# Kernel tuning notes

Measured on AMD Instinct MI355X. Metric: run time of the kernel, lower is better.

## Reference

```python
import jax, jax.numpy as jnp
import numpy as np

B, N, NF, DEG = 128, 1024, 64, 16
NH = 128          # top-level n_hidden
H = NH // 2       # per-branch hidden (64)
NNODES = B * N
NEDGES = NNODES * DEG
ANG = 2


def _lin(key, fi, fo):
    k1, k2 = jax.random.split(key)
    s = 1.0 / np.sqrt(fi)
    return (jax.random.uniform(k1, (fi, fo), minval=-s, maxval=s, dtype=jnp.float32),
            jax.random.uniform(k2, (fo,), minval=-s, maxval=s, dtype=jnp.float32))

_PARAM_DEFS = [("W_pre1_a", "b_pre1_a", NF, H), ("W_pre2_a", "b_pre2_a", H, H), ("W_gcn_a", "b_gcn_a", H, H),
               ("W_pre1_b", "b_pre1_b", NF, H), ("W_pre2_b", "b_pre2_b", H, H), ("W_gcn_b", "b_gcn_b", H, H),
               ("W_lin1", "b_lin1", 2 * NH + 1, NH), ("W_lin2", "b_lin2", NH, NH // 2),
               ("W_lin3", "b_lin3", NH // 2, 1), ("W_cb", "b_cb", NH // 2, 1),
               ("W_om", "b_om", NH // 2, ANG), ("W_th", "b_th", NH // 2, ANG), ("W_ph", "b_ph", NH // 2, ANG)]


def setup_inputs() -> dict:
    key = jax.random.key(0)
    ks = jax.random.split(key, 24)

    def edges(k):
        # block-structured edges: each graph g owns nodes [g*N, (g+1)*N)
        e = jax.random.randint(k, (2, NEDGES), 0, N, dtype=jnp.int32)
        off = (jnp.arange(NEDGES, dtype=jnp.int32) // (N * DEG)) * N
        return e + off[None, :]

    batch = jnp.arange(NNODES, dtype=jnp.int32) // N
    inp = {
        "x_a": jax.random.normal(ks[0], (NNODES, NF), dtype=jnp.float32),
        "edge_index_a": edges(ks[1]),
        "edge_attr_a": jax.random.uniform(ks[2], (NEDGES,), dtype=jnp.float32),
        "x_a_batch": batch,
        "x_b": jax.random.normal(ks[3], (NNODES, NF), dtype=jnp.float32),
        "edge_index_b": edges(ks[4]),
        "edge_attr_b": jax.random.uniform(ks[5], (NEDGES,), dtype=jnp.float32),
        "x_b_batch": batch,
        "linker_size": jax.random.uniform(ks[6], (B, 1), dtype=jnp.float32),
    }
    for i, (wn, bn, fi, fo) in enumerate(_PARAM_DEFS):
        w, b = _lin(ks[7 + i], fi, fo)
        inp[wn] = w
        inp[bn] = b
    return inp


def _gcn(x, W, b, src, dst, ew, n):
    # GCNConv with edge weights and self loops (fill_value=1):
    #   out = D^{-1/2} (A + I) D^{-1/2} (x W) + b
    h = x @ W
    deg = jax.ops.segment_sum(ew, dst, num_segments=n) + 1.0
    dinv = jax.lax.rsqrt(deg)
    norm = dinv[src] * ew * dinv[dst]                        # [E]
    out = jax.ops.segment_sum(h[src] * norm[:, None], dst, num_segments=n)
    out = out + h * (dinv * dinv)[:, None]                   # self-loop contribution
    return out + b


def _branch(x, ei, ea, bat, Wp1, bp1, Wp2, bp2, Wg, bg):
    x = jax.nn.relu(x @ Wp1 + bp1)
    x = jax.nn.relu(x @ Wp2 + bp2)
    x = jax.nn.relu(_gcn(x, Wg, bg, ei[0], ei[1], ea, x.shape[0]))
    s = jax.ops.segment_sum(x, bat, num_segments=B)          # gsp: global sum pool
    cnt = jax.ops.segment_sum(jnp.ones((x.shape[0], 1), x.dtype), bat, num_segments=B)
    return jnp.concatenate([s, s / cnt], axis=1)             # [B, 2H] = [gsp || gap(mean)]


def reference(x_a, edge_index_a, edge_attr_a, x_a_batch,
              x_b, edge_index_b, edge_attr_b, x_b_batch, linker_size,
              W_pre1_a, b_pre1_a, W_pre2_a, b_pre2_a, W_gcn_a, b_gcn_a,
              W_pre1_b, b_pre1_b, W_pre2_b, b_pre2_b, W_gcn_b, b_gcn_b,
              W_lin1, b_lin1, W_lin2, b_lin2, W_lin3, b_lin3,
              W_cb, b_cb, W_om, b_om, W_th, b_th, W_ph, b_ph):
    xa = _branch(x_a, edge_index_a, edge_attr_a, x_a_batch,
                 W_pre1_a, b_pre1_a, W_pre2_a, b_pre2_a, W_gcn_a, b_gcn_a)
    xb = _branch(x_b, edge_index_b, edge_attr_b, x_b_batch,
                 W_pre1_b, b_pre1_b, W_pre2_b, b_pre2_b, W_gcn_b, b_gcn_b)
    x = jnp.concatenate([xa, xb, linker_size], axis=1)       # [B, 2*NH+1]
    x = jax.nn.relu(x @ W_lin1 + b_lin1)                     # dropout p=0.0 -> identity
    x = jax.nn.relu(x @ W_lin2 + b_lin2)
    ca = x @ W_lin3 + b_lin3                                 # loss_type='bce' -> no sigmoid
    cb = x @ W_cb + b_cb
    om = x @ W_om + b_om
    th = x @ W_th + b_th
    ph = x @ W_ph + b_ph
    return (ca, cb, om, th, ph)
```

## Files before the change

kernel.cpp:

```cpp
#include <hip/hip_runtime.h>
#include <hip/hip_bf16.h>

#define NNODES 131072
#define NEDGES 2097152
#define NB     128
#define NPG    1024
#define EPG    16384

#define OFF_DEG      0
#define OFF_POOLED   (OFF_DEG + 2*NNODES)
#define OFF_WT       (OFF_POOLED + 2*NB*64)
#define OFF_H        (OFF_WT + 6*4096)
#define OFF_CNT      (OFF_H + (size_t)2*NNODES*64)
#define OFF_ROWSTART (OFF_CNT + 2*NNODES)
#define OFF_CURSOR   (OFF_ROWSTART + 2*NNODES)
#define OFF_CSR      (OFF_CURSOR + 2*NNODES)
#define WS_NEEDED    ((OFF_CSR + (size_t)4*NEDGES) * 4)

#define CSRB_LDS 145408

typedef __attribute__((ext_vector_type(8))) short bfrag;
typedef __attribute__((ext_vector_type(4))) float f32x4;

__device__ __forceinline__ unsigned short f2bf(float v) {
    unsigned int u = __float_as_uint(v);
    unsigned int r = (u + 0x7fffu + ((u >> 16) & 1u)) >> 16;
    return (unsigned short)r;
}
__device__ __forceinline__ float bf2f(unsigned short s) {
    return __uint_as_float(((unsigned int)s) << 16);
}
__device__ __forceinline__ float2 ntload2(const float2* p) {
    unsigned long long u = __builtin_nontemporal_load(
        reinterpret_cast<const unsigned long long*>(p));
    float2 r;
    r.x = __uint_as_float((unsigned int)(u & 0xffffffffu));
    r.y = __uint_as_float((unsigned int)(u >> 32));
    return r;
}

__global__ void wprep(const float* __restrict__ w0, const float* __restrict__ w1,
                      const float* __restrict__ w2, const float* __restrict__ w3,
                      const float* __restrict__ w4, const float* __restrict__ w5,
                      unsigned short* __restrict__ wf) {
    int m = blockIdx.x;
    const float* w = (m == 0) ? w0 : (m == 1) ? w1 : (m == 2) ? w2
                   : (m == 3) ? w3 : (m == 4) ? w4 : w5;
    for (int idx = threadIdx.x; idx < 4096; idx += blockDim.x) {
        int ft   = idx >> 10;
        int kt   = (idx >> 9) & 1;
        int lane = (idx >> 3) & 63;
        int i    = idx & 7;
        int f = ft * 16 + (lane & 15);
        int k = kt * 32 + ((lane >> 4) << 3) + i;
        float v = w[k * 64 + f];
        unsigned short hi = f2bf(v);
        unsigned short lo = f2bf(v - bf2f(hi));
        wf[m * 8192 + idx]        = hi;
        wf[m * 8192 + 4096 + idx] = lo;
    }
}

__global__ __launch_bounds__(512) void csr_build2(
    const int* __restrict__ eia, const float* __restrict__ eaa,
    const int* __restrict__ eib, const float* __restrict__ eab,
    float* __restrict__ deg, int* __restrict__ rowstart,
    int* __restrict__ cnt, float2* __restrict__ csr) {
    extern __shared__ char smem[];
    float2* scsr = (float2*)smem;
    float*  sdeg = (float*)(smem + 131072);
    int*    scnt = (int*)(smem + 135168);
    int*    scur = (int*)(smem + 139264);
    int*    sm   = (int*)(smem + 143360);
    const int g  = blockIdx.x;
    const int br = blockIdx.y;
    const int* ei   = br ? eib : eia;
    const float* ea = br ? eab : eaa;
    const int t     = threadIdx.x;
    const int ebase = g * EPG;
    const int nbase = g * NPG;

    for (int i = t; i < NPG; i += 512) { sdeg[i] = 0.f; scnt[i] = 0; }
    __syncthreads();

#pragma unroll 4
    for (int it = 0; it < EPG / 512; ++it) {
        int e = ebase + it * 512 + t;
        int d = ei[NEDGES + e] - nbase;
        float w = ea[e];
        atomicAdd(&scnt[d], 1);
        atomicAdd(&sdeg[d], w);
    }
    __syncthreads();

    for (int i = t; i < NPG; i += 512) {
        float dv = sdeg[i];
        deg[br * NNODES + nbase + i] = dv;
        sdeg[i] = rsqrtf(dv + 1.f);
    }

    int c0 = scnt[t * 2 + 0], c1 = scnt[t * 2 + 1];
    int T = c0 + c1;
    sm[t] = T;
    __syncthreads();
    for (int off = 1; off < 512; off <<= 1) {
        int v = (t >= off) ? sm[t - off] : 0;
        __syncthreads();
        sm[t] += v;
        __syncthreads();
    }
    int excl = sm[t] - T;
    int r0 = excl, r1 = excl + c0;
    int nout = br * NNODES + nbase + t * 2;
    rowstart[nout + 0] = ebase + r0;
    rowstart[nout + 1] = ebase + r1;
    cnt[nout + 0] = c0; cnt[nout + 1] = c1;
    scur[t * 2 + 0] = r0; scur[t * 2 + 1] = r1;
    __syncthreads();

#pragma unroll 4
    for (int it = 0; it < EPG / 512; ++it) {
        int e = ebase + it * 512 + t;
        int srcg = ei[e];
        int s = srcg - nbase;
        int d = ei[NEDGES + e] - nbase;
        float w = ea[e];
        int pos = atomicAdd(&scur[d], 1);
        float2 pr;
        pr.x = __int_as_float(srcg);
        pr.y = sdeg[s] * w * sdeg[d];
        scsr[pos] = pr;
    }
    __syncthreads();

    float4* dst4 = (float4*)(csr + (size_t)br * NEDGES + ebase);
    const float4* src4 = (const float4*)scsr;
    for (int i = t; i < 8192; i += 512) dst4[i] = src4[i];
}

__global__ __launch_bounds__(256) void csr_build(
    const int* __restrict__ eia, const float* __restrict__ eaa,
    const int* __restrict__ eib, const float* __restrict__ eab,
    float* __restrict__ deg, int* __restrict__ rowstart,
    int* __restrict__ cnt, float2* __restrict__ csr) {
    __shared__ float sdeg[NPG];
    __shared__ int   scnt[NPG];
    __shared__ int   scur[NPG];
    __shared__ int   sm[256];
    const int g  = blockIdx.x;
    const int br = blockIdx.y;
    const int* ei   = br ? eib : eia;
    const float* ea = br ? eab : eaa;
    const int t     = threadIdx.x;
    const int ebase = g * EPG;
    const int nbase = g * NPG;

    for (int i = t; i < NPG; i += 256) { sdeg[i] = 0.f; scnt[i] = 0; }
    __syncthreads();
#pragma unroll 4
    for (int it = 0; it < EPG / 256; ++it) {
        int e = ebase + it * 256 + t;
        int d = ei[NEDGES + e] - nbase;
        float w = ea[e];
        atomicAdd(&scnt[d], 1);
        atomicAdd(&sdeg[d], w);
    }
    __syncthreads();
    for (int i = t; i < NPG; i += 256) {
        float dv = sdeg[i];
        deg[br * NNODES + nbase + i] = dv;
        sdeg[i] = rsqrtf(dv + 1.f);
    }
    int c0 = scnt[t * 4 + 0], c1 = scnt[t * 4 + 1], c2 = scnt[t * 4 + 2], c3 = scnt[t * 4 + 3];
    int T = c0 + c1 + c2 + c3;
    sm[t] = T;
    __syncthreads();
    for (int off = 1; off < 256; off <<= 1) {
        int v = (t >= off) ? sm[t - off] : 0;
        __syncthreads();
        sm[t] += v;
        __syncthreads();
    }
    int excl = sm[t] - T;
    int base = ebase + excl;
    int r0 = base, r1 = base + c0, r2 = r1 + c1, r3 = r2 + c2;
    int nout = br * NNODES + nbase + t * 4;
    rowstart[nout + 0] = r0; rowstart[nout + 1] = r1;
    rowstart[nout + 2] = r2; rowstart[nout + 3] = r3;
    cnt[nout + 0] = c0; cnt[nout + 1] = c1; cnt[nout + 2] = c2; cnt[nout + 3] = c3;
    scur[t * 4 + 0] = r0; scur[t * 4 + 1] = r1;
    scur[t * 4 + 2] = r2; scur[t * 4 + 3] = r3;
    __syncthreads();
    float2* cso = csr + (size_t)br * NEDGES;
#pragma unroll 4
    for (int it = 0; it < EPG / 256; ++it) {
        int e = ebase + it * 256 + t;
        int srcg = ei[e];
        int s = srcg - nbase;
        int d = ei[NEDGES + e] - nbase;
        float w = ea[e];
        int pos = atomicAdd(&scur[d], 1);
        float2 pr;
        pr.x = __int_as_float(srcg);
        pr.y = sdeg[s] * w * sdeg[d];
        cso[pos] = pr;
    }
}

__global__ __launch_bounds__(256) void node_mlp_mfma(
    const float* __restrict__ xa, const float* __restrict__ xb,
    const unsigned short* __restrict__ wf,
    const float* __restrict__ b1a, const float* __restrict__ b2a,
    const float* __restrict__ b1b, const float* __restrict__ b2b,
    unsigned short* __restrict__ hout) {
    __shared__ float lds[4 * 16 * 65];
    const int br = blockIdx.y;
    const float* x = br ? xb : xa;
    const unsigned short* wfb = wf + br * 3 * 8192;
    const float* b1 = br ? b1b : b1a;
    const float* b2 = br ? b2b : b2a;
    const int wave = threadIdx.x >> 6;
    const int lane = threadIdx.x & 63;
    const int row  = lane & 15;
    const int kg   = lane >> 4;
    const int n0   = blockIdx.x * 64 + wave * 16;
    float* wlds = &lds[wave * 16 * 65];

    bfrag ahi[2], alo[2];
#pragma unroll
    for (int kt = 0; kt < 2; ++kt) {
        const float4* p = reinterpret_cast<const float4*>(
            x + (size_t)(n0 + row) * 64 + kt * 32 + kg * 8);
        float4 v0 = p[0], v1 = p[1];
        float vv[8] = {v0.x, v0.y, v0.z, v0.w, v1.x, v1.y, v1.z, v1.w};
        bfrag h, l;
#pragma unroll
        for (int i = 0; i < 8; ++i) {
            unsigned short hb = f2bf(vv[i]);
            unsigned short lb = f2bf(vv[i] - bf2f(hb));
            h[i] = (short)hb;
            l[i] = (short)lb;
        }
        ahi[kt] = h; alo[kt] = l;
    }

#pragma unroll
    for (int layer = 0; layer < 3; ++layer) {
        const unsigned short* wl = wfb + layer * 8192;
        bfrag bhi[4][2], blo[4][2];
#pragma unroll
        for (int ft = 0; ft < 4; ++ft)
#pragma unroll
            for (int kt = 0; kt < 2; ++kt) {
                bhi[ft][kt] = *reinterpret_cast<const bfrag*>(wl + ft * 1024 + kt * 512 + lane * 8);
                blo[ft][kt] = *reinterpret_cast<const bfrag*>(wl + 4096 + ft * 1024 + kt * 512 + lane * 8);
            }
        f32x4 acc[4];
#pragma unroll
        for (int ft = 0; ft < 4; ++ft) {
            float bv = (layer == 0) ? b1[ft * 16 + row]
                     : (layer == 1) ? b2[ft * 16 + row] : 0.f;
            acc[ft] = (f32x4){bv, bv, bv, bv};
        }
#pragma unroll
        for (int ft = 0; ft < 4; ++ft)
#pragma unroll
            for (int kt = 0; kt < 2; ++kt) {
                acc[ft] = __builtin_amdgcn_mfma_f32_16x16x32_bf16(ahi[kt], bhi[ft][kt], acc[ft], 0, 0, 0);
                acc[ft] = __builtin_amdgcn_mfma_f32_16x16x32_bf16(alo[kt], bhi[ft][kt], acc[ft], 0, 0, 0);
                acc[ft] = __builtin_amdgcn_mfma_f32_16x16x32_bf16(ahi[kt], blo[ft][kt], acc[ft], 0, 0, 0);
            }

        if (layer < 2) {
#pragma unroll
            for (int ft = 0; ft < 4; ++ft)
#pragma unroll
                for (int r = 0; r < 4; ++r)
                    wlds[(kg * 4 + r) * 65 + ft * 16 + row] = fmaxf(acc[ft][r], 0.f);
            __syncthreads();
#pragma unroll
            for (int kt = 0; kt < 2; ++kt) {
                const float* rp = &wlds[row * 65 + kt * 32 + kg * 8];
                bfrag h, l;
#pragma unroll
                for (int i = 0; i < 8; ++i) {
                    float v = rp[i];
                    unsigned short hb = f2bf(v);
                    unsigned short lb = f2bf(v - bf2f(hb));
                    h[i] = (short)hb;
                    l[i] = (short)lb;
                }
                ahi[kt] = h; alo[kt] = l;
            }
            __syncthreads();
        } else {
            unsigned short* hp = hout + (size_t)br * NNODES * 64 + (size_t)n0 * 64;
#pragma unroll
            for (int ft = 0; ft < 4; ++ft)
#pragma unroll
                for (int r = 0; r < 4; ++r)
                    hp[(kg * 4 + r) * 64 + ft * 16 + row] = f2bf(acc[ft][r]);
        }
    }
}

__global__ __launch_bounds__(256) void gcn_gather_pool(
    const int* __restrict__ rowstart, const int* __restrict__ cnt,
    const float2* __restrict__ csr, const float* __restrict__ deg,
    const unsigned short* __restrict__ h,
    const float* __restrict__ bga, const float* __restrict__ bgb,
    float* __restrict__ pooled) {
    __shared__ float red[256];
    const int bid  = blockIdx.x;
    const int xcd  = bid & 7;
    const int sub  = bid >> 3;
    const int gb   = xcd * 32 + (sub >> 4);
    const int blk  = sub & 15;
    const int br   = gb >> 7;
    const int g    = gb & 127;
    const int wave = threadIdx.x >> 6;
    const int lane = threadIdx.x & 63;
    const int n0   = g * NPG + blk * 64 + wave * 16;

    const int*    rs = rowstart + br * NNODES;
    const int*    ct = cnt + br * NNODES;
    const float2* cs = csr + (size_t)br * NEDGES;
    const float*  dg = deg + br * NNODES;
    const unsigned short* hh = h + (size_t)br * NNODES * 64;
    const float bias = (br ? bgb : bga)[lane];

    float psum = 0.f;
    for (int j = 0; j < 16; ++j) {
        int n = n0 + j;
        int r = __builtin_amdgcn_readfirstlane(rs[n]);
        int c = __builtin_amdgcn_readfirstlane(ct[n]);
        float s0 = 0.f, s1 = 0.f, s2 = 0.f, s3 = 0.f;
        float s4 = 0.f, s5 = 0.f, s6 = 0.f, s7 = 0.f;
        int i = 0;
        for (; i + 8 <= c; i += 8) {
            float2 p0 = ntload2(cs + r + i + 0);
            float2 p1 = ntload2(cs + r + i + 1);
            float2 p2 = ntload2(cs + r + i + 2);
            float2 p3 = ntload2(cs + r + i + 3);
            float2 p4 = ntload2(cs + r + i + 4);
            float2 p5 = ntload2(cs + r + i + 5);
            float2 p6 = ntload2(cs + r + i + 6);
            float2 p7 = ntload2(cs + r + i + 7);
            s0 = fmaf(p0.y, bf2f(hh[(size_t)__float_as_int(p0.x) * 64 + lane]), s0);
            s1 = fmaf(p1.y, bf2f(hh[(size_t)__float_as_int(p1.x) * 64 + lane]), s1);
            s2 = fmaf(p2.y, bf2f(hh[(size_t)__float_as_int(p2.x) * 64 + lane]), s2);
            s3 = fmaf(p3.y, bf2f(hh[(size_t)__float_as_int(p3.x) * 64 + lane]), s3);
            s4 = fmaf(p4.y, bf2f(hh[(size_t)__float_as_int(p4.x) * 64 + lane]), s4);
            s5 = fmaf(p5.y, bf2f(hh[(size_t)__float_as_int(p5.x) * 64 + lane]), s5);
            s6 = fmaf(p6.y, bf2f(hh[(size_t)__float_as_int(p6.x) * 64 + lane]), s6);
            s7 = fmaf(p7.y, bf2f(hh[(size_t)__float_as_int(p7.x) * 64 + lane]), s7);
        }
        for (; i + 4 <= c; i += 4) {
            float2 p0 = ntload2(cs + r + i + 0);
            float2 p1 = ntload2(cs + r + i + 1);
            float2 p2 = ntload2(cs + r + i + 2);
            float2 p3 = ntload2(cs + r + i + 3);
            s0 = fmaf(p0.y, bf2f(hh[(size_t)__float_as_int(p0.x) * 64 + lane]), s0);
            s1 = fmaf(p1.y, bf2f(hh[(size_t)__float_as_int(p1.x) * 64 + lane]), s1);
            s2 = fmaf(p2.y, bf2f(hh[(size_t)__float_as_int(p2.x) * 64 + lane]), s2);
            s3 = fmaf(p3.y, bf2f(hh[(size_t)__float_as_int(p3.x) * 64 + lane]), s3);
        }
        for (; i < c; ++i) {
            float2 p = ntload2(cs + r + i);
            s0 = fmaf(p.y, bf2f(hh[(size_t)__float_as_int(p.x) * 64 + lane]), s0);
        }
        float d = dg[n] + 1.f;
        float v = ((s0 + s1) + (s2 + s3)) + ((s4 + s5) + (s6 + s7))
                + bf2f(hh[(size_t)n * 64 + lane]) * (1.f / d) + bias;
        psum += fmaxf(v, 0.f);
    }
    red[threadIdx.x] = psum;
    __syncthreads();
    if (wave == 0) {
        float s = red[lane] + red[64 + lane] + red[128 + lane] + red[192 + lane];
        unsafeAtomicAdd(&pooled[br * (NB * 64) + g * 64 + lane], s);
    }
}

__global__ __launch_bounds__(128) void final_mlp(
    const float* __restrict__ pooled, const float* __restrict__ linker,
    const float* __restrict__ W1, const float* __restrict__ b1,
    const float* __restrict__ W2, const float* __restrict__ b2,
    const float* __restrict__ W3, const float* __restrict__ b3,
    const float* __restrict__ Wcb, const float* __restrict__ bcb,
    const float* __restrict__ Wom, const float* __restrict__ bom,
    const float* __restrict__ Wth, const float* __restrict__ bth,
    const float* __restrict__ Wph, const float* __restrict__ bph,
    float* __restrict__ out) {
    __shared__ float inv[260];
    __shared__ float x1[128];
    __shared__ float x2[64];
    const int g = blockIdx.x;
    const int t = threadIdx.x;
    if (t < 64) {
        float pa = pooled[g * 64 + t];
        float pb = pooled[NB * 64 + g * 64 + t];
        inv[t]       = pa;
        inv[64 + t]  = pa * (1.f / 1024.f);
        inv[128 + t] = pb;
        inv[192 + t] = pb * (1.f / 1024.f);
    }
    if (t == 0) inv[256] = linker[g];
    __syncthreads();

    {
        float a = b1[t];
        for (int i = 0; i < 257; ++i) a = fmaf(inv[i], W1[i * 128 + t], a);
        x1[t] = fmaxf(a, 0.f);
    }
    __syncthreads();
    if (t < 64) {
        float a = b2[t];
        for (int i = 0; i < 128; ++i) a = fmaf(x1[i], W2[i * 64 + t], a);
        x2[t] = fmaxf(a, 0.f);
    }
    __syncthreads();
    if (t < 8) {
        if (t == 0) {
            float a = b3[0];
            for (int i = 0; i < 64; ++i) a = fmaf(x2[i], W3[i], a);
            out[g] = a;
        } else if (t == 1) {
            float a = bcb[0];
            for (int i = 0; i < 64; ++i) a = fmaf(x2[i], Wcb[i], a);
            out[128 + g] = a;
        } else if (t < 4) {
            int j = t - 2; float a = bom[j];
            for (int i = 0; i < 64; ++i) a = fmaf(x2[i], Wom[i * 2 + j], a);
            out[256 + g * 2 + j] = a;
        } else if (t < 6) {
            int j = t - 4; float a = bth[j];
            for (int i = 0; i < 64; ++i) a = fmaf(x2[i], Wth[i * 2 + j], a);
            out[512 + g * 2 + j] = a;
        } else {
            int j = t - 6; float a = bph[j];
            for (int i = 0; i < 64; ++i) a = fmaf(x2[i], Wph[i * 2 + j], a);
            out[768 + g * 2 + j] = a;
        }
    }
}

extern "C" void kernel_launch(void* const* d_in, const int* in_sizes, int n_in,
                              void* d_out, int out_size, void* d_ws, size_t ws_size,
                              hipStream_t stream) {
    const float* x_a  = (const float*)d_in[0];
    const int*   ei_a = (const int*)d_in[1];
    const float* ea_a = (const float*)d_in[2];
    const float* x_b  = (const float*)d_in[4];
    const int*   ei_b = (const int*)d_in[5];
    const float* ea_b = (const float*)d_in[6];
    const float* linker = (const float*)d_in[8];
    const float* W_pre1_a = (const float*)d_in[9];
    const float* b_pre1_a = (const float*)d_in[10];
    const float* W_pre2_a = (const float*)d_in[11];
    const float* b_pre2_a = (const float*)d_in[12];
    const float* W_gcn_a  = (const float*)d_in[13];
    const float* b_gcn_a  = (const float*)d_in[14];
    const float* W_pre1_b = (const float*)d_in[15];
    const float* b_pre1_b = (const float*)d_in[16];
    const float* W_pre2_b = (const float*)d_in[17];
    const float* b_pre2_b = (const float*)d_in[18];
    const float* W_gcn_b  = (const float*)d_in[19];
    const float* b_gcn_b  = (const float*)d_in[20];
    const float* W_lin1 = (const float*)d_in[21];
    const float* b_lin1 = (const float*)d_in[22];
    const float* W_lin2 = (const float*)d_in[23];
    const float* b_lin2 = (const float*)d_in[24];
    const float* W_lin3 = (const float*)d_in[25];
    const float* b_lin3 = (const float*)d_in[26];
    const float* W_cb = (const float*)d_in[27];
    const float* b_cb = (const float*)d_in[28];
    const float* W_om = (const float*)d_in[29];
    const float* b_om = (const float*)d_in[30];
    const float* W_th = (const float*)d_in[31];
    const float* b_th = (const float*)d_in[32];
    const float* W_ph = (const float*)d_in[33];
    const float* b_ph = (const float*)d_in[34];

    float* ws     = (float*)d_ws;
    float* deg    = ws + OFF_DEG;
    float* pooled = ws + OFF_POOLED;
    float* wtw    = ws + OFF_WT;
    unsigned short* h = (unsigned short*)(ws + OFF_H);
    int*   cnt      = (int*)(ws + OFF_CNT);
    int*   rowstart = (int*)(ws + OFF_ROWSTART);
    float2* csr     = (float2*)(ws + OFF_CSR);

    hipMemsetAsync(pooled, 0, 2 * NB * 64 * sizeof(float), stream);
    wprep<<<6, 256, 0, stream>>>(W_pre1_a, W_pre2_a, W_gcn_a,
                                 W_pre1_b, W_pre2_b, W_gcn_b,
                                 (unsigned short*)wtw);

    hipError_t attr_ok = hipFuncSetAttribute(
        reinterpret_cast<const void*>(&csr_build2),
        hipFuncAttributeMaxDynamicSharedMemorySize, CSRB_LDS);
    if (attr_ok == hipSuccess) {
        csr_build2<<<dim3(NB, 2), 512, CSRB_LDS, stream>>>(ei_a, ea_a, ei_b, ea_b,
                                                           deg, rowstart, cnt, csr);
    } else {
        csr_build<<<dim3(NB, 2), 256, 0, stream>>>(ei_a, ea_a, ei_b, ea_b,
                                                   deg, rowstart, cnt, csr);
    }

    node_mlp_mfma<<<dim3(NNODES / 64, 2), 256, 0, stream>>>(
        x_a, x_b, (const unsigned short*)wtw,
        b_pre1_a, b_pre2_a, b_pre1_b, b_pre2_b, h);
    gcn_gather_pool<<<4096, 256, 0, stream>>>(rowstart, cnt, csr, deg, h,
                                              b_gcn_a, b_gcn_b, pooled);

    final_mlp<<<NB, 128, 0, stream>>>(pooled, linker,
                                      W_lin1, b_lin1, W_lin2, b_lin2, W_lin3, b_lin3,
                                      W_cb, b_cb, W_om, b_om, W_th, b_th, W_ph, b_ph,
                                      (float*)d_out);
}
```

Before: 379.2 us.

## Fuse CSR build with GCN gather-pool in one LDS-resident kernel per graph

Merges per-graph CSR construction and GCN aggregation/pooling into one kernel. The CSR stays in LDS instead of being written to and re-read from global memory, which also removes the deg/rowstart/cnt writes and the pooled memset and atomics. The cost is parallelism: the gather now runs on only 256 blocks of 512 threads instead of 4096 blocks, which may limit latency hiding for the random h gathers. The fallback gather path is also trimmed to 4-way unrolling with plain loads.

```diff
diff --git a/kernel.cpp b/kernel.cpp
--- a/kernel.cpp
+++ b/kernel.cpp
@@ -17,7 +17,7 @@
 #define OFF_CSR      (OFF_CURSOR + 2*NNODES)
 #define WS_NEEDED    ((OFF_CSR + (size_t)4*NEDGES) * 4)
 
-#define CSRB_LDS 145408
+#define FUSE_LDS 145408
 
 typedef __attribute__((ext_vector_type(8))) short bfrag;
 typedef __attribute__((ext_vector_type(4))) float f32x4;
@@ -29,14 +29,6 @@
 }
 __device__ __forceinline__ float bf2f(unsigned short s) {
     return __uint_as_float(((unsigned int)s) << 16);
-}
-__device__ __forceinline__ float2 ntload2(const float2* p) {
-    unsigned long long u = __builtin_nontemporal_load(
-        reinterpret_cast<const unsigned long long*>(p));
-    float2 r;
-    r.x = __uint_as_float((unsigned int)(u & 0xffffffffu));
-    r.y = __uint_as_float((unsigned int)(u >> 32));
-    return r;
 }
 
 __global__ void wprep(const float* __restrict__ w0, const float* __restrict__ w1,
@@ -61,17 +53,19 @@
     }
 }
 
-__global__ __launch_bounds__(512) void csr_build2(
+__global__ __launch_bounds__(512) void csr_gcn_fused(
     const int* __restrict__ eia, const float* __restrict__ eaa,
     const int* __restrict__ eib, const float* __restrict__ eab,
-    float* __restrict__ deg, int* __restrict__ rowstart,
-    int* __restrict__ cnt, float2* __restrict__ csr) {
+    const unsigned short* __restrict__ h,
+    const float* __restrict__ bga, const float* __restrict__ bgb,
+    float* __restrict__ pooled) {
     extern __shared__ char smem[];
     float2* scsr = (float2*)smem;
     float*  sdeg = (float*)(smem + 131072);
     int*    scnt = (int*)(smem + 135168);
     int*    scur = (int*)(smem + 139264);
     int*    sm   = (int*)(smem + 143360);
+    float*  red  = (float*)sm;
     const int g  = blockIdx.x;
     const int br = blockIdx.y;
     const int* ei   = br ? eib : eia;
@@ -93,11 +87,7 @@
     }
     __syncthreads();
 
-    for (int i = t; i < NPG; i += 512) {
-        float dv = sdeg[i];
-        deg[br * NNODES + nbase + i] = dv;
-        sdeg[i] = rsqrtf(dv + 1.f);
-    }
+    for (int i = t; i < NPG; i += 512) sdeg[i] = rsqrtf(sdeg[i] + 1.f);
 
     int c0 = scnt[t * 2 + 0], c1 = scnt[t * 2 + 1];
     int T = c0 + c1;
@@ -110,12 +100,8 @@
         __syncthreads();
     }
     int excl = sm[t] - T;
-    int r0 = excl, r1 = excl + c0;
-    int nout = br * NNODES + nbase + t * 2;
-    rowstart[nout + 0] = ebase + r0;
-    rowstart[nout + 1] = ebase + r1;
-    cnt[nout + 0] = c0; cnt[nout + 1] = c1;
-    scur[t * 2 + 0] = r0; scur[t * 2 + 1] = r1;
+    scur[t * 2 + 0] = excl;
+    scur[t * 2 + 1] = excl + c0;
     __syncthreads();
 
 #pragma unroll 4
@@ -133,9 +119,65 @@
     }
     __syncthreads();
 
-    float4* dst4 = (float4*)(csr + (size_t)br * NEDGES + ebase);
-    const float4* src4 = (const float4*)scsr;
-    for (int i = t; i < 8192; i += 512) dst4[i] = src4[i];
+    const unsigned short* hh = h + (size_t)br * NNODES * 64;
+    const int wave = t >> 6;
+    const int lane = t & 63;
+    const float bias = (br ? bgb : bga)[lane];
+
+    float psum = 0.f;
+    for (int j = 0; j < 128; ++j) {
+        int n = wave * 128 + j;
+        int end = __builtin_amdgcn_readfirstlane(scur[n]);
+        int c   = __builtin_amdgcn_readfirstlane(scnt[n]);
+        int r   = end - c;
+        float s0 = 0.f, s1 = 0.f, s2 = 0.f, s3 = 0.f;
+        float s4 = 0.f, s5 = 0.f, s6 = 0.f, s7 = 0.f;
+        int i = 0;
+        for (; i + 8 <= c; i += 8) {
+            float2 p0 = scsr[r + i + 0];
+            float2 p1 = scsr[r + i + 1];
+            float2 p2 = scsr[r + i + 2];
+            float2 p3 = scsr[r + i + 3];
+            float2 p4 = scsr[r + i + 4];
+            float2 p5 = scsr[r + i + 5];
+            float2 p6 = scsr[r + i + 6];
+            float2 p7 = scsr[r + i + 7];
+            s0 = fmaf(p0.y, bf2f(hh[(size_t)__float_as_int(p0.x) * 64 + lane]), s0);
+            s1 = fmaf(p1.y, bf2f(hh[(size_t)__float_as_int(p1.x) * 64 + lane]), s1);
+            s2 = fmaf(p2.y, bf2f(hh[(size_t)__float_as_int(p2.x) * 64 + lane]), s2);
+            s3 = fmaf(p3.y, bf2f(hh[(size_t)__float_as_int(p3.x) * 64 + lane]), s3);
+            s4 = fmaf(p4.y, bf2f(hh[(size_t)__float_as_int(p4.x) * 64 + lane]), s4);
+            s5 = fmaf(p5.y, bf2f(hh[(size_t)__float_as_int(p5.x) * 64 + lane]), s5);
+            s6 = fmaf(p6.y, bf2f(hh[(size_t)__float_as_int(p6.x) * 64 + lane]), s6);
+            s7 = fmaf(p7.y, bf2f(hh[(size_t)__float_as_int(p7.x) * 64 + lane]), s7);
+        }
+        for (; i + 4 <= c; i += 4) {
+            float2 p0 = scsr[r + i + 0];
+            float2 p1 = scsr[r + i + 1];
+            float2 p2 = scsr[r + i + 2];
+            float2 p3 = scsr[r + i + 3];
+            s0 = fmaf(p0.y, bf2f(hh[(size_t)__float_as_int(p0.x) * 64 + lane]), s0);
+            s1 = fmaf(p1.y, bf2f(hh[(size_t)__float_as_int(p1.x) * 64 + lane]), s1);
+            s2 = fmaf(p2.y, bf2f(hh[(size_t)__float_as_int(p2.x) * 64 + lane]), s2);
+            s3 = fmaf(p3.y, bf2f(hh[(size_t)__float_as_int(p3.x) * 64 + lane]), s3);
+        }
+        for (; i < c; ++i) {
+            float2 p = scsr[r + i];
+            s0 = fmaf(p.y, bf2f(hh[(size_t)__float_as_int(p.x) * 64 + lane]), s0);
+        }
+        float dinv = sdeg[n];
+        float v = ((s0 + s1) + (s2 + s3)) + ((s4 + s5) + (s6 + s7))
+                + bf2f(hh[(size_t)(nbase + n) * 64 + lane]) * dinv * dinv + bias;
+        psum += fmaxf(v, 0.f);
+    }
+    red[t] = psum;
+    __syncthreads();
+    if (wave == 0) {
+        float s = 0.f;
+#pragma unroll
+        for (int w2 = 0; w2 < 8; ++w2) s += red[w2 * 64 + lane];
+        pooled[br * (NB * 64) + g * 64 + lane] = s;
+    }
 }
 
 __global__ __launch_bounds__(256) void csr_build(
@@ -335,42 +377,23 @@
         int r = __builtin_amdgcn_readfirstlane(rs[n]);
         int c = __builtin_amdgcn_readfirstlane(ct[n]);
         float s0 = 0.f, s1 = 0.f, s2 = 0.f, s3 = 0.f;
-        float s4 = 0.f, s5 = 0.f, s6 = 0.f, s7 = 0.f;
         int i = 0;
-        for (; i + 8 <= c; i += 8) {
-            float2 p0 = ntload2(cs + r + i + 0);
-            float2 p1 = ntload2(cs + r + i + 1);
-            float2 p2 = ntload2(cs + r + i + 2);
-            float2 p3 = ntload2(cs + r + i + 3);
-            float2 p4 = ntload2(cs + r + i + 4);
-            float2 p5 = ntload2(cs + r + i + 5);
-            float2 p6 = ntload2(cs + r + i + 6);
-            float2 p7 = ntload2(cs + r + i + 7);
+        for (; i + 4 <= c; i += 4) {
+            float2 p0 = cs[r + i + 0];
+            float2 p1 = cs[r + i + 1];
+            float2 p2 = cs[r + i + 2];
+            float2 p3 = cs[r + i + 3];
             s0 = fmaf(p0.y, bf2f(hh[(size_t)__float_as_int(p0.x) * 64 + lane]), s0);
             s1 = fmaf(p1.y, bf2f(hh[(size_t)__float_as_int(p1.x) * 64 + lane]), s1);
             s2 = fmaf(p2.y, bf2f(hh[(size_t)__float_as_int(p2.x) * 64 + lane]), s2);
             s3 = fmaf(p3.y, bf2f(hh[(size_t)__float_as_int(p3.x) * 64 + lane]), s3);
-            s4 = fmaf(p4.y, bf2f(hh[(size_t)__float_as_int(p4.x) * 64 + lane]), s4);
-            s5 = fmaf(p5.y, bf2f(hh[(size_t)__float_as_int(p5.x) * 64 + lane]), s5);
-            s6 = fmaf(p6.y, bf2f(hh[(size_t)__float_as_int(p6.x) * 64 + lane]), s6);
-            s7 = fmaf(p7.y, bf2f(hh[(size_t)__float_as_int(p7.x) * 64 + lane]), s7);
-        }
-        for (; i + 4 <= c; i += 4) {
-            float2 p0 = ntload2(cs + r + i + 0);
-            float2 p1 = ntload2(cs + r + i + 1);
-            float2 p2 = ntload2(cs + r + i + 2);
-            float2 p3 = ntload2(cs + r + i + 3);
-            s0 = fmaf(p0.y, bf2f(hh[(size_t)__float_as_int(p0.x) * 64 + lane]), s0);
-            s1 = fmaf(p1.y, bf2f(hh[(size_t)__float_as_int(p1.x) * 64 + lane]), s1);
-            s2 = fmaf(p2.y, bf2f(hh[(size_t)__float_as_int(p2.x) * 64 + lane]), s2);
-            s3 = fmaf(p3.y, bf2f(hh[(size_t)__float_as_int(p3.x) * 64 + lane]), s3);
         }
         for (; i < c; ++i) {
-            float2 p = ntload2(cs + r + i);
+            float2 p = cs[r + i];
             s0 = fmaf(p.y, bf2f(hh[(size_t)__float_as_int(p.x) * 64 + lane]), s0);
         }
         float d = dg[n] + 1.f;
-        float v = ((s0 + s1) + (s2 + s3)) + ((s4 + s5) + (s6 + s7))
+        float v = (s0 + s1) + (s2 + s3)
                 + bf2f(hh[(size_t)n * 64 + lane]) * (1.f / d) + bias;
         psum += fmaxf(v, 0.f);
     }
@@ -491,27 +514,26 @@
     int*   rowstart = (int*)(ws + OFF_ROWSTART);
     float2* csr     = (float2*)(ws + OFF_CSR);
 
-    hipMemsetAsync(pooled, 0, 2 * NB * 64 * sizeof(float), stream);
     wprep<<<6, 256, 0, stream>>>(W_pre1_a, W_pre2_a, W_gcn_a,
                                  W_pre1_b, W_pre2_b, W_gcn_b,
                                  (unsigned short*)wtw);
-
-    hipError_t attr_ok = hipFuncSetAttribute(
-        reinterpret_cast<const void*>(&csr_build2),
-        hipFuncAttributeMaxDynamicSharedMemorySize, CSRB_LDS);
-    if (attr_ok == hipSuccess) {
-        csr_build2<<<dim3(NB, 2), 512, CSRB_LDS, stream>>>(ei_a, ea_a, ei_b, ea_b,
-                                                           deg, rowstart, cnt, csr);
-    } else {
-        csr_build<<<dim3(NB, 2), 256, 0, stream>>>(ei_a, ea_a, ei_b, ea_b,
-                                                   deg, rowstart, cnt, csr);
-    }
-
     node_mlp_mfma<<<dim3(NNODES / 64, 2), 256, 0, stream>>>(
         x_a, x_b, (const unsigned short*)wtw,
         b_pre1_a, b_pre2_a, b_pre1_b, b_pre2_b, h);
-    gcn_gather_pool<<<4096, 256, 0, stream>>>(rowstart, cnt, csr, deg, h,
-                                              b_gcn_a, b_gcn_b, pooled);
+
+    hipError_t attr_ok = hipFuncSetAttribute(
+        reinterpret_cast<const void*>(&csr_gcn_fused),
+        hipFuncAttributeMaxDynamicSharedMemorySize, FUSE_LDS);
+    if (attr_ok == hipSuccess) {
+        csr_gcn_fused<<<dim3(NB, 2), 512, FUSE_LDS, stream>>>(
+            ei_a, ea_a, ei_b, ea_b, h, b_gcn_a, b_gcn_b, pooled);
+    } else {
+        hipMemsetAsync(pooled, 0, 2 * NB * 64 * sizeof(float), stream);
+        csr_build<<<dim3(NB, 2), 256, 0, stream>>>(ei_a, ea_a, ei_b, ea_b,
+                                                   deg, rowstart, cnt, csr);
+        gcn_gather_pool<<<4096, 256, 0, stream>>>(rowstart, cnt, csr, deg, h,
+                                                  b_gcn_a, b_gcn_b, pooled);
+    }
 
     final_mlp<<<NB, 128, 0, stream>>>(pooled, linker,
                                       W_lin1, b_lin1, W_lin2, b_lin2, W_lin3, b_lin3,
```

New measurement: 448.5 us. 18.3% more time.
